# Performance work log

Measured on AMD Instinct MI355X. Metric: run time of the kernel, lower is better.

## Reference

```python
import jax, jax.numpy as jnp
import numpy as np

EMBED_DIM = 1024
NUM_HEADS = 16
SEQ = 2048
BATCH = 2


def setup_inputs() -> dict:
    key = jax.random.key(0)
    ks = jax.random.split(key, 9)
    E = EMBED_DIM
    gain = 1.0 / np.sqrt(2.0)  # xavier_uniform with gain 1/sqrt(2) (qkv_same_dim)
    limit = gain * np.sqrt(6.0 / (E + E))
    q = jax.random.normal(ks[0], (SEQ, BATCH, E), dtype=jnp.float32)
    k = jax.random.normal(ks[1], (SEQ, BATCH, E), dtype=jnp.float32)
    v = jax.random.normal(ks[2], (SEQ, BATCH, E), dtype=jnp.float32)
    Wq = jax.random.uniform(ks[3], (E, E), jnp.float32, -limit, limit)
    Wk = jax.random.uniform(ks[4], (E, E), jnp.float32, -limit, limit)
    Wv = jax.random.uniform(ks[5], (E, E), jnp.float32, -limit, limit)
    bq = jnp.zeros((E,), jnp.float32)
    bk = jnp.zeros((E,), jnp.float32)
    bv = jnp.zeros((E,), jnp.float32)
    return {"query": q, "key": k, "value": v,
            "Wq": Wq, "bq": bq, "Wk": Wk, "bk": bk, "Wv": Wv, "bv": bv}


def reference(query, key, value, Wq, bq, Wk, bk, Wv, bv):
    # Base Taylor attention path (norm_taylor=True, do_scale=True, has_out=False).
    L, B, E = query.shape
    H = NUM_HEADS
    hd = E // H
    scaling = E ** (-0.5)  # self.scaling = dim**-0.5, dim == embed_dim

    q = (query @ Wq + bq) * scaling          # (L, B, E)
    k = key @ Wk + bk                         # (S, B, E)
    v = value @ Wv + bv                       # (S, B, E)

    def split_heads(x):
        # (T, B, E) -> (B*H, T, hd)
        T = x.shape[0]
        return x.reshape(T, B * H, hd).transpose(1, 0, 2)

    qh, kh, vh = split_heads(q), split_heads(k), split_heads(v)

    # Taylor expansion of exp(qk) to first order: 1 + q.k
    attn = 1.0 + jnp.einsum('bld,bsd->bls', qh, kh)   # (B*H, L, S)
    attn = attn / attn.sum(axis=-1, keepdims=True)    # row-normalize
    out = jnp.einsum('bls,bsd->bld', attn, vh)        # (B*H, L, hd)
    out = out.transpose(1, 0, 2).reshape(L, B, E)     # (L, B, E)
    return out
```

## Files before the change

### kernel.cpp

```cpp
#include <hip/hip_runtime.h>
#include <hip/hip_bf16.h>

#define L_SEQ 2048
#define BATCH 2
#define ROWS 4096
#define E 1024
#define NH 16
#define HD 64

typedef __attribute__((ext_vector_type(4))) float f32x4;
typedef __attribute__((ext_vector_type(8))) __bf16 bf16x8;

#define SWZ(byt) ((byt) ^ ((((byt) >> 7) & 7) << 4))

__device__ __forceinline__ void gload16(const void* g, void* l) {
    __builtin_amdgcn_global_load_lds((const __attribute__((address_space(1))) void*)g,
                                     (__attribute__((address_space(3))) void*)l,
                                     16, 0, 0);
}

__global__ __launch_bounds__(256) void prep(const float* __restrict__ q,
                                            const float* __restrict__ k,
                                            const float* __restrict__ v,
                                            const float* __restrict__ Wq,
                                            const float* __restrict__ Wk,
                                            const float* __restrict__ Wv,
                                            __bf16* __restrict__ Xb,
                                            __bf16* __restrict__ Wt) {
    const int z = blockIdx.y;
    if (blockIdx.x < 2048) {
        const float* src = (z == 0) ? q : ((z == 1) ? k : v);
        __bf16* dst = Xb + (size_t)z * ROWS * E;
        const size_t i = ((size_t)blockIdx.x * 256 + threadIdx.x) * 8;
        const float4 a = *(const float4*)(src + i);
        const float4 b = *(const float4*)(src + i + 4);
        bf16x8 o;
        o[0] = (__bf16)a.x; o[1] = (__bf16)a.y; o[2] = (__bf16)a.z; o[3] = (__bf16)a.w;
        o[4] = (__bf16)b.x; o[5] = (__bf16)b.y; o[6] = (__bf16)b.z; o[7] = (__bf16)b.w;
        *(bf16x8*)(dst + i) = o;
        return;
    }
    const float* W = (z == 0) ? Wq : ((z == 1) ? Wk : Wv);
    __bf16* dst = Wt + (size_t)z * E * E;
    __shared__ __align__(16) float t[64][65];
    const int tt = blockIdx.x - 2048;
    const int n0 = (tt & 15) * 64, k0 = (tt >> 4) * 64;
    const int r = threadIdx.x >> 2, c4 = threadIdx.x & 3;
#pragma unroll
    for (int j = 0; j < 4; ++j) {
        const float4 vv = *(const float4*)&W[(size_t)(k0 + r) * E + n0 + c4 * 16 + j * 4];
        t[r][c4 * 16 + j * 4 + 0] = vv.x;
        t[r][c4 * 16 + j * 4 + 1] = vv.y;
        t[r][c4 * 16 + j * 4 + 2] = vv.z;
        t[r][c4 * 16 + j * 4 + 3] = vv.w;
    }
    __syncthreads();
    bf16x8 o0, o1;
#pragma unroll
    for (int j = 0; j < 8; ++j) {
        o0[j] = (__bf16)t[c4 * 16 + j][r];
        o1[j] = (__bf16)t[c4 * 16 + 8 + j][r];
    }
    *(bf16x8*)&dst[(size_t)(n0 + r) * E + k0 + c4 * 16] = o0;
    *(bf16x8*)&dst[(size_t)(n0 + r) * E + k0 + c4 * 16 + 8] = o1;
}

__device__ __forceinline__ void stage_tile(const __bf16* __restrict__ gsrc, int row0, int kcol,
                                           char* ldsdst, int wv, int ln) {
#pragma unroll
    for (int r = 0; r < 4; ++r) {
        const int rowg = row0 + r * 32 + wv * 8 + (ln >> 3);
        const int c16 = (ln & 7) ^ (ln >> 3);
        gload16(gsrc + (size_t)rowg * E + kcol + c16 * 8,
                ldsdst + r * 4096 + wv * 1024);
    }
}

__device__ __forceinline__ bf16x8 fragld(const char* base, int row, int kk, int kg) {
    return *(const bf16x8*)(base + row * 128 + ((((kk << 2) | kg) ^ (row & 7)) << 4));
}

#define PH_SYNC_BEGIN  __builtin_amdgcn_s_barrier(); \
                       asm volatile("s_waitcnt lgkmcnt(0)" ::: "memory"); \
                       __builtin_amdgcn_s_setprio(1);
#define PH_SYNC_END    __builtin_amdgcn_s_setprio(0); \
                       __builtin_amdgcn_s_barrier();

__global__ __launch_bounds__(256, 2) void gemm_qkv(const __bf16* __restrict__ Xb,
                                                   const __bf16* __restrict__ Wt,
                                                   const float* __restrict__ bq,
                                                   const float* __restrict__ bk,
                                                   const float* __restrict__ bv,
                                                   __bf16* __restrict__ Cb) {
    __shared__ __align__(16) char smem[65536];
    const int z = blockIdx.z;
    const __bf16* A = Xb + (size_t)z * ROWS * E;
    const __bf16* B = Wt + (size_t)z * E * E;
    __bf16* C = Cb + (size_t)z * ROWS * E;
    const float* bias = (z == 0) ? bq : ((z == 1) ? bk : bv);
    const float alpha = (z == 0) ? 0.03125f : 1.0f;
    const int m0 = blockIdx.y * 128, n0 = blockIdx.x * 128;
    const int tid = threadIdx.x, ln = tid & 63, wv = tid >> 6;
    const int lr = ln & 15, kg = ln >> 4;
    const int wm = (wv & 1) * 64, wn = (wv >> 1) * 64;
    char* LA0 = smem;            char* LA1 = smem + 16384;
    char* LB0 = smem + 32768;    char* LB1 = smem + 49152;

    stage_tile(A, m0, 0,  LA0, wv, ln);
    stage_tile(B, n0, 0,  LB0, wv, ln);
    stage_tile(A, m0, 64, LA1, wv, ln);
    asm volatile("s_waitcnt vmcnt(4)" ::: "memory");
    __builtin_amdgcn_s_barrier();

    f32x4 acc[4][4] = {};
    bf16x8 Af[4][2], Bf[2][2];

#define LOAD_B(nb) \
    _Pragma("unroll") for (int nn = 0; nn < 2; ++nn) \
    _Pragma("unroll") for (int kk = 0; kk < 2; ++kk) \
        Bf[nn][kk] = fragld(cB, wn + ((nb) + nn) * 16 + lr, kk, kg);
#define QUAD(q) \
    _Pragma("unroll") for (int m = 0; m < 4; ++m) \
    _Pragma("unroll") for (int nn = 0; nn < 2; ++nn) \
    _Pragma("unroll") for (int kk = 0; kk < 2; ++kk) \
        acc[m][2 * (q) + nn] = __builtin_amdgcn_mfma_f32_16x16x32_bf16(Af[m][kk], Bf[nn][kk], acc[m][2 * (q) + nn], 0, 0, 0);

    for (int T = 0; T < 16; ++T) {
        const char* cA = (T & 1) ? LA1 : LA0;
        const char* cB = (T & 1) ? LB1 : LB0;
        char* nB = (T & 1) ? LB0 : LB1;
        char* nA = (T & 1) ? LA1 : LA0;
#pragma unroll
        for (int m = 0; m < 4; ++m)
#pragma unroll
            for (int kk = 0; kk < 2; ++kk)
                Af[m][kk] = fragld(cA, wm + m * 16 + lr, kk, kg);
        LOAD_B(0);
        if (T < 15) stage_tile(B, n0, (T + 1) * 64, nB, wv, ln);
        PH_SYNC_BEGIN; QUAD(0); PH_SYNC_END;
        LOAD_B(2);
        if (T < 14) stage_tile(A, m0, (T + 2) * 64, nA, wv, ln);
        PH_SYNC_BEGIN; QUAD(1);
        __builtin_amdgcn_s_setprio(0);
        if (T < 14)       { asm volatile("s_waitcnt vmcnt(4)" ::: "memory"); }
        else if (T == 14) { asm volatile("s_waitcnt vmcnt(0)" ::: "memory"); }
        __builtin_amdgcn_s_barrier();
    }
#undef LOAD_B
#undef QUAD

#pragma unroll
    for (int m = 0; m < 4; ++m) {
        const int rbase = m0 + wm + m * 16 + kg * 4;
#pragma unroll
        for (int n = 0; n < 4; ++n) {
            const int col = n0 + wn + n * 16 + lr;
            const float bcol = bias[col];
#pragma unroll
            for (int rr = 0; rr < 4; ++rr)
                C[(size_t)(rbase + rr) * E + col] = (__bf16)((acc[m][n][rr] + bcol) * alpha);
        }
    }
}

__global__ __launch_bounds__(256) void reduce_kv(const __bf16* __restrict__ Kb,
                                                 const __bf16* __restrict__ Vb,
                                                 float* __restrict__ Mpart,
                                                 float* __restrict__ ksumP,
                                                 float* __restrict__ vsumP) {
    const int bh = blockIdx.x, b = bh >> 4, h = bh & 15;
    const int ts = blockIdx.y;
    const int t0 = ts * 128;
    __shared__ __align__(16) __bf16 sK[128 * 64];
    __shared__ __align__(16) __bf16 sV[128 * 64];
    __shared__ float red_k[4][64];
    __shared__ float red_v[4][64];
    const int tid = threadIdx.x;
    const int lane = tid & 63, wave = tid >> 6;
    const int lr = lane & 15, kg = lane >> 4;

    float vk[8] = {}, vv[8] = {};
    const int d0 = (tid & 7) * 8;
#pragma unroll
    for (int i = 0; i < 4; ++i) {
        const int t = i * 32 + (tid >> 3);
        const size_t g = (size_t)((t0 + t) * 2 + b) * E + h * 64 + d0;
        const bf16x8 kv = *(const bf16x8*)&Kb[g];
        const bf16x8 vvv = *(const bf16x8*)&Vb[g];
        const int lo = (t * 128 + d0 * 2) ^ (wave << 5);
        *(bf16x8*)((char*)sK + lo) = kv;
        *(bf16x8*)((char*)sV + lo) = vvv;
#pragma unroll
        for (int j = 0; j < 8; ++j) { vk[j] += (float)kv[j]; vv[j] += (float)vvv[j]; }
    }
#pragma unroll
    for (int m = 8; m <= 32; m <<= 1)
#pragma unroll
        for (int j = 0; j < 8; ++j) {
            vk[j] += __shfl_xor(vk[j], m, 64);
            vv[j] += __shfl_xor(vv[j], m, 64);
        }
    if (lane < 8)
#pragma unroll
        for (int j = 0; j < 8; ++j) {
            red_k[wave][lane * 8 + j] = vk[j];
            red_v[wave][lane * 8 + j] = vv[j];
        }
    __syncthreads();

    f32x4 acc[4] = {};
#pragma unroll
    for (int kt = 0; kt < 4; ++kt) {
        const int tb = kt * 32;
        bf16x8 afr, bfr[4];
        const char* pv = (const char*)sV + (((tb + kg * 8) * 128 + (wave * 16 + lr) * 2) ^ (kg << 5));
#pragma unroll
        for (int j = 0; j < 8; ++j) afr[j] = *(const __bf16*)(pv + j * 128);
#pragma unroll
        for (int ni = 0; ni < 4; ++ni) {
            const char* pk = (const char*)sK + (((tb + kg * 8) * 128 + (ni * 16 + lr) * 2) ^ (kg << 5));
#pragma unroll
            for (int j = 0; j < 8; ++j) bfr[ni][j] = *(const __bf16*)(pk + j * 128);
        }
#pragma unroll
        for (int ni = 0; ni < 4; ++ni)
            acc[ni] = __builtin_amdgcn_mfma_f32_16x16x32_bf16(afr, bfr[ni], acc[ni], 0, 0, 0);
    }

    float* Mp = Mpart + ((size_t)bh * 16 + ts) * 4096;
#pragma unroll
    for (int ni = 0; ni < 4; ++ni)
#pragma unroll
        for (int rr = 0; rr < 4; ++rr)
            Mp[(wave * 16 + kg * 4 + rr) * 64 + ni * 16 + lr] = acc[ni][rr];
    if (tid < 64)
        ksumP[(bh * 16 + ts) * 64 + tid] = red_k[0][tid] + red_k[1][tid] + red_k[2][tid] + red_k[3][tid];
    else if (tid < 128) {
        const int d = tid - 64;
        vsumP[(bh * 16 + ts) * 64 + d] = red_v[0][d] + red_v[1][d] + red_v[2][d] + red_v[3][d];
    }
}

__global__ __launch_bounds__(256) void combine_m(const float* __restrict__ Mpart,
                                                 const float* __restrict__ ksumP,
                                                 const float* __restrict__ vsumP,
                                                 float* __restrict__ Mt,
                                                 float* __restrict__ ksum,
                                                 float* __restrict__ vsum) {
    const int blk = blockIdx.x, tid = threadIdx.x;
    if (blk < 256) {
        const int e2 = (blk * 256 + tid) * 2;
        const int bh = e2 >> 12, r = e2 & 4095;
        const float* src = Mpart + (size_t)bh * 16 * 4096 + r;
        float s0 = 0.f, s1 = 0.f;
#pragma unroll
        for (int ts = 0; ts < 16; ++ts) {
            s0 += src[ts * 4096];
            s1 += src[ts * 4096 + 1];
        }
        Mt[(size_t)bh * 4096 + r] = s0;
        Mt[(size_t)bh * 4096 + r + 1] = s1;
    } else if (blk < 264) {
        const int idx = (blk - 256) * 256 + tid;
        const int bh = idx >> 6, d = idx & 63;
        float s = 0.f;
#pragma unroll
        for (int ts = 0; ts < 16; ++ts) s += ksumP[bh * 1024 + ts * 64 + d];
        ksum[idx] = s;
    } else {
        const int idx = (blk - 264) * 256 + tid;
        const int bh = idx >> 6, d = idx & 63;
        float s = 0.f;
#pragma unroll
        for (int ts = 0; ts < 16; ++ts) s += vsumP[bh * 1024 + ts * 64 + d];
        vsum[idx] = s;
    }
}

__global__ __launch_bounds__(256) void taylor_out(const __bf16* __restrict__ Qb,
                                                  const float* __restrict__ Mt,
                                                  const float* __restrict__ ksum,
                                                  const float* __restrict__ vsum,
                                                  float* __restrict__ out) {
    const int b = blockIdx.y;
    const int lblk = blockIdx.x * 16;
    const int tid = threadIdx.x, lane = tid & 63, wave = tid >> 6;
    const int lr = lane & 15, kg = lane >> 4;
    __shared__ __align__(16) __bf16 sM[4][4096];
    for (int hh = 0; hh < 4; ++hh) {
        __syncthreads();
#pragma unroll
        for (int i = 0; i < 8; ++i) {
            const int idx = i * 256 + tid;
            const int hseg = idx >> 9, rem = idx & 511;
            const float* src = &Mt[(size_t)(b * 16 + hseg * 4 + hh) * 4096 + rem * 8];
            const float4 mA = *(const float4*)src;
            const float4 mB = *(const float4*)(src + 4);
            bf16x8 o;
            o[0] = (__bf16)mA.x; o[1] = (__bf16)mA.y; o[2] = (__bf16)mA.z; o[3] = (__bf16)mA.w;
            o[4] = (__bf16)mB.x; o[5] = (__bf16)mB.y; o[6] = (__bf16)mB.z; o[7] = (__bf16)mB.w;
            *(bf16x8*)((char*)&sM[hseg][0] + SWZ(rem * 16)) = o;
        }
        __syncthreads();
        const int h = wave * 4 + hh;
        const int bh = b * 16 + h;
        const int rA = (lblk + lr) * 2 + b;
        const bf16x8 a0 = *(const bf16x8*)&Qb[(size_t)rA * E + h * 64 + kg * 8];
        const bf16x8 a1 = *(const bf16x8*)&Qb[(size_t)rA * E + h * 64 + 32 + kg * 8];
        float p = 0.f;
        const float* ks = &ksum[bh * 64];
#pragma unroll
        for (int j = 0; j < 8; ++j)
            p += (float)a0[j] * ks[kg * 8 + j] + (float)a1[j] * ks[32 + kg * 8 + j];
        p += __shfl_xor(p, 16, 64);
        p += __shfl_xor(p, 32, 64);
        const float Z = 2048.0f + p;
        f32x4 acc[4] = {};
#pragma unroll
        for (int ni = 0; ni < 4; ++ni) {
            const int byt0 = (ni * 16 + lr) * 128 + kg * 16;
            const bf16x8 b0 = *(const bf16x8*)((const char*)&sM[wave][0] + SWZ(byt0));
            const bf16x8 b1 = *(const bf16x8*)((const char*)&sM[wave][0] + SWZ(byt0 + 64));
            acc[ni] = __builtin_amdgcn_mfma_f32_16x16x32_bf16(a0, b0, acc[ni], 0, 0, 0);
            acc[ni] = __builtin_amdgcn_mfma_f32_16x16x32_bf16(a1, b1, acc[ni], 0, 0, 0);
        }
        float invZ[4];
#pragma unroll
        for (int rr = 0; rr < 4; ++rr) invZ[rr] = 1.0f / __shfl(Z, kg * 4 + rr, 64);
        const float* vs = &vsum[bh * 64];
#pragma unroll
        for (int ni = 0; ni < 4; ++ni)
#pragma unroll
            for (int rr = 0; rr < 4; ++rr) {
                const int l_out = lblk + kg * 4 + rr;
                out[(size_t)(l_out * 2 + b) * E + h * 64 + ni * 16 + lr] =
                    (vs[ni * 16 + lr] + acc[ni][rr]) * invZ[rr];
            }
    }
}

extern "C" void kernel_launch(void* const* d_in, const int* in_sizes, int n_in,
                              void* d_out, int out_size, void* d_ws, size_t ws_size,
                              hipStream_t stream) {
    const float* q  = (const float*)d_in[0];
    const float* k  = (const float*)d_in[1];
    const float* v  = (const float*)d_in[2];
    const float* Wq = (const float*)d_in[3];
    const float* bq = (const float*)d_in[4];
    const float* Wk = (const float*)d_in[5];
    const float* bk = (const float*)d_in[6];
    const float* Wv = (const float*)d_in[7];
    const float* bv = (const float*)d_in[8];
    float* out = (float*)d_out;
    char* w = (char*)d_ws;
    __bf16* Xb = (__bf16*)(w);
    __bf16* Wt = (__bf16*)(w + 25165824);
    __bf16* Cb = (__bf16*)(w + 31457280);
    float* Mt   = (float*)(w + 56623104);
    float* ksum = (float*)(w + 57147392);
    float* vsum = (float*)(w + 57155584);
    float* Mpart = (float*)(w);
    float* ksumP = (float*)(w + 8388608);
    float* vsumP = (float*)(w + 8519680);

    prep<<<dim3(2304, 3), 256, 0, stream>>>(q, k, v, Wq, Wk, Wv, Xb, Wt);
    gemm_qkv<<<dim3(8, 32, 3), 256, 0, stream>>>(Xb, Wt, bq, bk, bv, Cb);
    reduce_kv<<<dim3(32, 16), 256, 0, stream>>>(Cb + (size_t)ROWS * E,
                                                Cb + 2 * (size_t)ROWS * E, Mpart, ksumP, vsumP);
    combine_m<<<272, 256, 0, stream>>>(Mpart, ksumP, vsumP, Mt, ksum, vsum);
    taylor_out<<<dim3(128, 2), 256, 0, stream>>>(Cb, Mt, ksum, vsum, out);
}
```

Before: 82.27 us.

## Fuse fp32-to-bf16 activation conversion into QKV GEMM A-tile loads

Drops the separate conversion pass over q/k/v. The GEMM now loads fp32 activations straight into registers, converts them to bf16 and writes them into LDS, while B goes through a triple-buffered LDS pipeline in 80KB of dynamic shared memory. The grid is transposed so M is the fastest block index, and the workspace is re-laid out. This removes a full write and read of the bf16 activations, at the cost of twice the global bytes per A tile and more registers, and the larger LDS may reduce occupancy.

```diff
diff --git a/kernel.cpp b/kernel.cpp
--- a/kernel.cpp
+++ b/kernel.cpp
@@ -19,32 +19,15 @@
                                      16, 0, 0);
 }
 
-__global__ __launch_bounds__(256) void prep(const float* __restrict__ q,
-                                            const float* __restrict__ k,
-                                            const float* __restrict__ v,
-                                            const float* __restrict__ Wq,
-                                            const float* __restrict__ Wk,
-                                            const float* __restrict__ Wv,
-                                            __bf16* __restrict__ Xb,
-                                            __bf16* __restrict__ Wt) {
-    const int z = blockIdx.y;
-    if (blockIdx.x < 2048) {
-        const float* src = (z == 0) ? q : ((z == 1) ? k : v);
-        __bf16* dst = Xb + (size_t)z * ROWS * E;
-        const size_t i = ((size_t)blockIdx.x * 256 + threadIdx.x) * 8;
-        const float4 a = *(const float4*)(src + i);
-        const float4 b = *(const float4*)(src + i + 4);
-        bf16x8 o;
-        o[0] = (__bf16)a.x; o[1] = (__bf16)a.y; o[2] = (__bf16)a.z; o[3] = (__bf16)a.w;
-        o[4] = (__bf16)b.x; o[5] = (__bf16)b.y; o[6] = (__bf16)b.z; o[7] = (__bf16)b.w;
-        *(bf16x8*)(dst + i) = o;
-        return;
-    }
+__global__ __launch_bounds__(256) void prep_w(const float* __restrict__ Wq,
+                                              const float* __restrict__ Wk,
+                                              const float* __restrict__ Wv,
+                                              __bf16* __restrict__ Wt) {
+    const int z = blockIdx.z;
     const float* W = (z == 0) ? Wq : ((z == 1) ? Wk : Wv);
     __bf16* dst = Wt + (size_t)z * E * E;
     __shared__ __align__(16) float t[64][65];
-    const int tt = blockIdx.x - 2048;
-    const int n0 = (tt & 15) * 64, k0 = (tt >> 4) * 64;
+    const int n0 = blockIdx.x * 64, k0 = blockIdx.y * 64;
     const int r = threadIdx.x >> 2, c4 = threadIdx.x & 3;
 #pragma unroll
     for (int j = 0; j < 4; ++j) {
@@ -65,8 +48,8 @@
     *(bf16x8*)&dst[(size_t)(n0 + r) * E + k0 + c4 * 16 + 8] = o1;
 }
 
-__device__ __forceinline__ void stage_tile(const __bf16* __restrict__ gsrc, int row0, int kcol,
-                                           char* ldsdst, int wv, int ln) {
+__device__ __forceinline__ void stageB(const __bf16* __restrict__ gsrc, int row0, int kcol,
+                                       char* ldsdst, int wv, int ln) {
 #pragma unroll
     for (int r = 0; r < 4; ++r) {
         const int rowg = row0 + r * 32 + wv * 8 + (ln >> 3);
@@ -76,44 +59,75 @@
     }
 }
 
+__device__ __forceinline__ void loadA_f32(const float* __restrict__ gsrc, int row0, int kcol,
+                                          float4 (&o)[4][2], int wv, int ln) {
+#pragma unroll
+    for (int r = 0; r < 4; ++r) {
+        const int rowg = row0 + r * 32 + wv * 8 + (ln >> 3);
+        const int c16 = (ln & 7) ^ (ln >> 3);
+        const float* p = gsrc + (size_t)rowg * E + kcol + c16 * 8;
+        o[r][0] = *(const float4*)p;
+        o[r][1] = *(const float4*)(p + 4);
+    }
+}
+
+__device__ __forceinline__ void writeA_lds(const float4 (&a)[4][2], char* dst, int wv, int ln) {
+#pragma unroll
+    for (int r = 0; r < 4; ++r) {
+        bf16x8 o;
+        o[0] = (__bf16)a[r][0].x; o[1] = (__bf16)a[r][0].y;
+        o[2] = (__bf16)a[r][0].z; o[3] = (__bf16)a[r][0].w;
+        o[4] = (__bf16)a[r][1].x; o[5] = (__bf16)a[r][1].y;
+        o[6] = (__bf16)a[r][1].z; o[7] = (__bf16)a[r][1].w;
+        *(bf16x8*)(dst + r * 4096 + wv * 1024 + ln * 16) = o;
+    }
+}
+
 __device__ __forceinline__ bf16x8 fragld(const char* base, int row, int kk, int kg) {
     return *(const bf16x8*)(base + row * 128 + ((((kk << 2) | kg) ^ (row & 7)) << 4));
 }
 
 #define PH_SYNC_BEGIN  __builtin_amdgcn_s_barrier(); \
                        asm volatile("s_waitcnt lgkmcnt(0)" ::: "memory"); \
+                       __builtin_amdgcn_sched_barrier(0); \
                        __builtin_amdgcn_s_setprio(1);
 #define PH_SYNC_END    __builtin_amdgcn_s_setprio(0); \
                        __builtin_amdgcn_s_barrier();
 
-__global__ __launch_bounds__(256, 2) void gemm_qkv(const __bf16* __restrict__ Xb,
+__global__ __launch_bounds__(256, 2) void gemm_qkv(const float* __restrict__ xq,
+                                                   const float* __restrict__ xk,
+                                                   const float* __restrict__ xv,
                                                    const __bf16* __restrict__ Wt,
                                                    const float* __restrict__ bq,
                                                    const float* __restrict__ bk,
                                                    const float* __restrict__ bv,
                                                    __bf16* __restrict__ Cb) {
-    __shared__ __align__(16) char smem[65536];
+    extern __shared__ __align__(16) char smem[];
     const int z = blockIdx.z;
-    const __bf16* A = Xb + (size_t)z * ROWS * E;
+    const float* A = (z == 0) ? xq : ((z == 1) ? xk : xv);
     const __bf16* B = Wt + (size_t)z * E * E;
     __bf16* C = Cb + (size_t)z * ROWS * E;
     const float* bias = (z == 0) ? bq : ((z == 1) ? bk : bv);
     const float alpha = (z == 0) ? 0.03125f : 1.0f;
-    const int m0 = blockIdx.y * 128, n0 = blockIdx.x * 128;
+    const int m0 = blockIdx.x * 128, n0 = blockIdx.y * 128;
     const int tid = threadIdx.x, ln = tid & 63, wv = tid >> 6;
     const int lr = ln & 15, kg = ln >> 4;
     const int wm = (wv & 1) * 64, wn = (wv >> 1) * 64;
-    char* LA0 = smem;            char* LA1 = smem + 16384;
-    char* LB0 = smem + 32768;    char* LB1 = smem + 49152;
-
-    stage_tile(A, m0, 0,  LA0, wv, ln);
-    stage_tile(B, n0, 0,  LB0, wv, ln);
-    stage_tile(A, m0, 64, LA1, wv, ln);
-    asm volatile("s_waitcnt vmcnt(4)" ::: "memory");
+
+    stageB(B, n0, 0,  smem + 32768, wv, ln);
+    stageB(B, n0, 64, smem + 49152, wv, ln);
+    float4 a0r[4][2], a1r[4][2];
+    loadA_f32(A, m0, 0,  a0r, wv, ln);
+    loadA_f32(A, m0, 64, a1r, wv, ln);
+    asm volatile("s_waitcnt vmcnt(16)" ::: "memory");
+    writeA_lds(a0r, smem,        wv, ln);
+    writeA_lds(a1r, smem + 16384, wv, ln);
+    asm volatile("s_waitcnt lgkmcnt(0)" ::: "memory");
     __builtin_amdgcn_s_barrier();
 
     f32x4 acc[4][4] = {};
     bf16x8 Af[4][2], Bf[2][2];
+    float4 areg[4][2];
 
 #define LOAD_B(nb) \
     _Pragma("unroll") for (int nn = 0; nn < 2; ++nn) \
@@ -126,25 +140,26 @@
         acc[m][2 * (q) + nn] = __builtin_amdgcn_mfma_f32_16x16x32_bf16(Af[m][kk], Bf[nn][kk], acc[m][2 * (q) + nn], 0, 0, 0);
 
     for (int T = 0; T < 16; ++T) {
-        const char* cA = (T & 1) ? LA1 : LA0;
-        const char* cB = (T & 1) ? LB1 : LB0;
-        char* nB = (T & 1) ? LB0 : LB1;
-        char* nA = (T & 1) ? LA1 : LA0;
+        const char* cA = smem + (T & 1) * 16384;
+        const char* cB = smem + 32768 + (T % 3) * 16384;
+        char* nA = smem + (T & 1) * 16384;
+        char* nB = smem + 32768 + ((T + 2) % 3) * 16384;
+        if (T < 14) {
+            loadA_f32(A, m0, (T + 2) * 64, areg, wv, ln);
+            stageB(B, n0, (T + 2) * 64, nB, wv, ln);
+        }
 #pragma unroll
         for (int m = 0; m < 4; ++m)
 #pragma unroll
             for (int kk = 0; kk < 2; ++kk)
                 Af[m][kk] = fragld(cA, wm + m * 16 + lr, kk, kg);
         LOAD_B(0);
-        if (T < 15) stage_tile(B, n0, (T + 1) * 64, nB, wv, ln);
         PH_SYNC_BEGIN; QUAD(0); PH_SYNC_END;
-        LOAD_B(2);
-        if (T < 14) stage_tile(A, m0, (T + 2) * 64, nA, wv, ln);
-        PH_SYNC_BEGIN; QUAD(1);
-        __builtin_amdgcn_s_setprio(0);
         if (T < 14)       { asm volatile("s_waitcnt vmcnt(4)" ::: "memory"); }
         else if (T == 14) { asm volatile("s_waitcnt vmcnt(0)" ::: "memory"); }
-        __builtin_amdgcn_s_barrier();
+        if (T < 14) writeA_lds(areg, nA, wv, ln);
+        LOAD_B(2);
+        PH_SYNC_BEGIN; QUAD(1); PH_SYNC_END;
     }
 #undef LOAD_B
 #undef QUAD
@@ -353,18 +368,19 @@
     const float* bv = (const float*)d_in[8];
     float* out = (float*)d_out;
     char* w = (char*)d_ws;
-    __bf16* Xb = (__bf16*)(w);
-    __bf16* Wt = (__bf16*)(w + 25165824);
-    __bf16* Cb = (__bf16*)(w + 31457280);
-    float* Mt   = (float*)(w + 56623104);
-    float* ksum = (float*)(w + 57147392);
-    float* vsum = (float*)(w + 57155584);
-    float* Mpart = (float*)(w);
-    float* ksumP = (float*)(w + 8388608);
-    float* vsumP = (float*)(w + 8519680);
-
-    prep<<<dim3(2304, 3), 256, 0, stream>>>(q, k, v, Wq, Wk, Wv, Xb, Wt);
-    gemm_qkv<<<dim3(8, 32, 3), 256, 0, stream>>>(Xb, Wt, bq, bk, bv, Cb);
+    __bf16* Wt = (__bf16*)(w);
+    __bf16* Cb = (__bf16*)(w + 6291456);
+    float* Mt    = (float*)(w + 31457280);
+    float* ksum  = (float*)(w + 31981568);
+    float* vsum  = (float*)(w + 31989760);
+    float* Mpart = (float*)(w + 31997952);
+    float* ksumP = (float*)(w + 40386560);
+    float* vsumP = (float*)(w + 40517632);
+
+    hipFuncSetAttribute((const void*)gemm_qkv,
+                        hipFuncAttributeMaxDynamicSharedMemorySize, 81920);
+    prep_w<<<dim3(16, 16, 3), 256, 0, stream>>>(Wq, Wk, Wv, Wt);
+    gemm_qkv<<<dim3(32, 8, 3), 256, 81920, stream>>>(q, k, v, Wt, bq, bk, bv, Cb);
     reduce_kv<<<dim3(32, 16), 256, 0, stream>>>(Cb + (size_t)ROWS * E,
                                                 Cb + 2 * (size_t)ROWS * E, Mpart, ksumP, vsumP);
     combine_m<<<272, 256, 0, stream>>>(Mpart, ksumP, vsumP, Mt, ksum, vsum);
```

New measurement: 88.21 us. 7.2% more time.
